# Kernel tuning notes

Hardware: AMD Instinct MI355X
Metric: run time of the kernel (lower is better)

Reference implementation:

```python
import jax, jax.numpy as jnp
import numpy as np

B, N = 4096, 1024


def setup_inputs() -> dict:
    key = jax.random.key(0)
    k1, k2 = jax.random.split(key)
    cors = 0.1 * jax.random.normal(k1, (B, N, 3), dtype=jnp.float32)  # predicted correspondences/offsets
    p_src = jax.random.normal(k2, (B, N, 3), dtype=jnp.float32)       # source point cloud
    return {"cors": cors, "p_src": p_src}


def reference(cors, p_src):
    # p_pred = p_src + cors  (target points implied by correspondences)
    p_pred = p_src + cors
    # centroids over the point dimension: [B, 1, 3]
    src_centroid = jnp.mean(p_src, axis=1, keepdims=True)
    pred_centroid = jnp.mean(p_pred, axis=1, keepdims=True)
    src_trans = p_src - src_centroid
    pred_trans = p_pred - pred_centroid
    # 3x3 cross-covariance per batch: h = src_trans^T @ pred_trans  -> [B, 3, 3]
    h = jnp.einsum('bnd,bne->bde', src_trans, pred_trans)
    # tf.linalg.svd returns s, u, v with h = u diag(s) v^T; jnp returns u, s, vh with vh = v^T
    u, s, vh = jnp.linalg.svd(h, full_matrices=False)
    # r_est = v @ u^T = (u @ vh)^T
    r_est = jnp.swapaxes(jnp.matmul(u, vh), -1, -2)  # [B, 3, 3]
    # t_est = -r_est @ src_centroid^T + pred_centroid^T  -> [B, 3, 1]
    t_est = -jnp.matmul(r_est, jnp.swapaxes(src_centroid, -1, -2)) + jnp.swapaxes(pred_centroid, -1, -2)
    g_top = jnp.concatenate([r_est, t_est], axis=2)  # [B, 3, 4]
    last_row = jnp.broadcast_to(
        jnp.array([[[0.0, 0.0, 0.0, 1.0]]], dtype=g_top.dtype), (g_top.shape[0], 1, 4)
    )
    return jnp.concatenate([g_top, last_row], axis=1)  # [B, 4, 4]
```

## Files before the change

### kernel.cpp

```cpp
#include <hip/hip_runtime.h>


constexpr int NPTS    = 1024;
constexpr int THREADS = 256;

__global__ __launch_bounds__(THREADS) void svd_layer_kernel(
    const float* __restrict__ cors,
    const float* __restrict__ p_src,
    float* __restrict__ out)
{
    const int b   = blockIdx.x;
    const int tid = threadIdx.x;
    const size_t base = (size_t)b * NPTS * 3;

    const float4* src4 = reinterpret_cast<const float4*>(p_src + base);
    const float4* cor4 = reinterpret_cast<const float4*>(cors  + base);
    float4 s0 = src4[tid*3+0], s1 = src4[tid*3+1], s2 = src4[tid*3+2];
    float4 c0 = cor4[tid*3+0], c1 = cor4[tid*3+1], c2 = cor4[tid*3+2];

    float sx[4] = {s0.x, s0.w, s1.z, s2.y};
    float sy[4] = {s0.y, s1.x, s1.w, s2.z};
    float sz[4] = {s0.z, s1.y, s2.x, s2.w};
    float px[4] = {sx[0]+c0.x, sx[1]+c0.w, sx[2]+c1.z, sx[3]+c2.y};
    float py[4] = {sy[0]+c0.y, sy[1]+c1.x, sy[2]+c1.w, sy[3]+c2.z};
    float pz[4] = {sz[0]+c0.z, sz[1]+c1.y, sz[2]+c2.x, sz[3]+c2.w};

    float acc[15];
    #pragma unroll
    for (int i = 0; i < 15; ++i) acc[i] = 0.f;
    #pragma unroll
    for (int k = 0; k < 4; ++k) {
        acc[0]  += sx[k]; acc[1]  += sy[k]; acc[2]  += sz[k];
        acc[3]  += px[k]; acc[4]  += py[k]; acc[5]  += pz[k];
        acc[6]  += sx[k]*px[k]; acc[7]  += sx[k]*py[k]; acc[8]  += sx[k]*pz[k];
        acc[9]  += sy[k]*px[k]; acc[10] += sy[k]*py[k]; acc[11] += sy[k]*pz[k];
        acc[12] += sz[k]*px[k]; acc[13] += sz[k]*py[k]; acc[14] += sz[k]*pz[k];
    }

    #pragma unroll
    for (int off = 32; off > 0; off >>= 1) {
        #pragma unroll
        for (int i = 0; i < 15; ++i) acc[i] += __shfl_down(acc[i], off, 64);
    }

    __shared__ float red[4][15];
    const int wave = tid >> 6, lane = tid & 63;
    if (lane == 0) {
        #pragma unroll
        for (int i = 0; i < 15; ++i) red[wave][i] = acc[i];
    }
    __syncthreads();
    if (tid != 0) return;

    double S[15];
    #pragma unroll
    for (int i = 0; i < 15; ++i)
        S[i] = (double)red[0][i] + (double)red[1][i] + (double)red[2][i] + (double)red[3][i];

    const double invN = 1.0 / (double)NPTS;
    double cs[3] = {S[0]*invN, S[1]*invN, S[2]*invN};
    double cp[3] = {S[3]*invN, S[4]*invN, S[5]*invN};

    double H[3][3];
    for (int i = 0; i < 3; ++i)
        for (int j = 0; j < 3; ++j)
            H[i][j] = S[6 + i*3 + j] - (double)NPTS * cs[i] * cp[j];

    double A[3][3];
    for (int i = 0; i < 3; ++i)
        for (int j = 0; j < 3; ++j) {
            double v = 0.0;
            for (int k = 0; k < 3; ++k) v += H[k][i] * H[k][j];
            A[i][j] = v;
        }

    double V[3][3] = {{1,0,0},{0,1,0},{0,0,1}};
    for (int sweep = 0; sweep < 8; ++sweep) {
        for (int pi = 0; pi < 3; ++pi) {
            const int p = (pi == 2) ? 1 : 0;
            const int q = (pi == 0) ? 1 : 2;
            const double apq = A[p][q];
            if (fabs(apq) < 1e-300) continue;
            const double tau = (A[q][q] - A[p][p]) / (2.0 * apq);
            const double t   = ((tau >= 0.0) ? 1.0 : -1.0) /
                               (fabs(tau) + sqrt(1.0 + tau*tau));
            const double c   = 1.0 / sqrt(1.0 + t*t);
            const double s   = t * c;
            A[p][p] -= t * apq;
            A[q][q] += t * apq;
            A[p][q] = A[q][p] = 0.0;
            const int k = 3 - p - q;
            const double akp = A[k][p], akq = A[k][q];
            A[k][p] = A[p][k] = c*akp - s*akq;
            A[k][q] = A[q][k] = s*akp + c*akq;
            for (int r = 0; r < 3; ++r) {
                const double vrp = V[r][p], vrq = V[r][q];
                V[r][p] = c*vrp - s*vrq;
                V[r][q] = s*vrp + c*vrq;
            }
        }
    }

    double inv[3];
    for (int i = 0; i < 3; ++i) {
        double w = A[i][i] > 0.0 ? A[i][i] : 0.0;
        double sv = sqrt(w);
        inv[i] = (sv > 1e-12) ? 1.0 / sv : 0.0;
    }
    double M[3][3];
    for (int i = 0; i < 3; ++i)
        for (int j = 0; j < 3; ++j) {
            double v = 0.0;
            for (int k = 0; k < 3; ++k) v += V[i][k] * inv[k] * V[j][k];
            M[i][j] = v;
        }

    double R[3][3];
    for (int i = 0; i < 3; ++i)
        for (int j = 0; j < 3; ++j) {
            double v = 0.0;
            for (int k = 0; k < 3; ++k) v += M[i][k] * H[j][k];
            R[i][j] = v;
        }
    double tt[3];
    for (int i = 0; i < 3; ++i)
        tt[i] = cp[i] - (R[i][0]*cs[0] + R[i][1]*cs[1] + R[i][2]*cs[2]);

    float* o = out + (size_t)b * 16;
    o[0]  = (float)R[0][0]; o[1]  = (float)R[0][1]; o[2]  = (float)R[0][2]; o[3]  = (float)tt[0];
    o[4]  = (float)R[1][0]; o[5]  = (float)R[1][1]; o[6]  = (float)R[1][2]; o[7]  = (float)tt[1];
    o[8]  = (float)R[2][0]; o[9]  = (float)R[2][1]; o[10] = (float)R[2][2]; o[11] = (float)tt[2];
    o[12] = 0.f; o[13] = 0.f; o[14] = 0.f; o[15] = 1.f;
}

extern "C" void kernel_launch(void* const* d_in, const int* in_sizes, int n_in,
                              void* d_out, int out_size, void* d_ws, size_t ws_size,
                              hipStream_t stream)
{
    const float* cors  = (const float*)d_in[0];
    const float* p_src = (const float*)d_in[1];
    float* out = (float*)d_out;
    const int B = in_sizes[0] / (NPTS * 3);
    hipLaunchKernelGGL(svd_layer_kernel, dim3(B), dim3(THREADS), 0, stream,
                       cors, p_src, out);
}
```

Baseline: 127.5 us.

## Map one batch per wavefront and replace Jacobi SVD with Newton-Schulz polar iteration

```diff
diff --git a/kernel.cpp b/kernel.cpp
--- a/kernel.cpp
+++ b/kernel.cpp
@@ -1,40 +1,53 @@
 #include <hip/hip_runtime.h>
 
 
-constexpr int NPTS    = 1024;
-constexpr int THREADS = 256;
+constexpr int NPTS  = 1024;
+constexpr int WAVES = 4;
+constexpr int THREADS = WAVES * 64;
 
 __global__ __launch_bounds__(THREADS) void svd_layer_kernel(
     const float* __restrict__ cors,
     const float* __restrict__ p_src,
-    float* __restrict__ out)
+    float* __restrict__ out,
+    int B)
 {
-    const int b   = blockIdx.x;
-    const int tid = threadIdx.x;
-    const size_t base = (size_t)b * NPTS * 3;
+    const int wave = threadIdx.x >> 6;
+    const int lane = threadIdx.x & 63;
+    const int b    = blockIdx.x * WAVES + wave;
+    if (b >= B) return;
 
-    const float4* src4 = reinterpret_cast<const float4*>(p_src + base);
-    const float4* cor4 = reinterpret_cast<const float4*>(cors  + base);
-    float4 s0 = src4[tid*3+0], s1 = src4[tid*3+1], s2 = src4[tid*3+2];
-    float4 c0 = cor4[tid*3+0], c1 = cor4[tid*3+1], c2 = cor4[tid*3+2];
+    const size_t base4 = (size_t)b * (NPTS * 3 / 4);
+    const float4* s4 = reinterpret_cast<const float4*>(p_src) + base4 + lane * 12;
+    const float4* c4 = reinterpret_cast<const float4*>(cors)  + base4 + lane * 12;
 
-    float sx[4] = {s0.x, s0.w, s1.z, s2.y};
-    float sy[4] = {s0.y, s1.x, s1.w, s2.z};
-    float sz[4] = {s0.z, s1.y, s2.x, s2.w};
-    float px[4] = {sx[0]+c0.x, sx[1]+c0.w, sx[2]+c1.z, sx[3]+c2.y};
-    float py[4] = {sy[0]+c0.y, sy[1]+c1.x, sy[2]+c1.w, sy[3]+c2.z};
-    float pz[4] = {sz[0]+c0.z, sz[1]+c1.y, sz[2]+c2.x, sz[3]+c2.w};
+    float4 sv[12], cv[12];
+    #pragma unroll
+    for (int m = 0; m < 12; ++m) sv[m] = s4[m];
+    #pragma unroll
+    for (int m = 0; m < 12; ++m) cv[m] = c4[m];
 
     float acc[15];
     #pragma unroll
     for (int i = 0; i < 15; ++i) acc[i] = 0.f;
+
     #pragma unroll
-    for (int k = 0; k < 4; ++k) {
-        acc[0]  += sx[k]; acc[1]  += sy[k]; acc[2]  += sz[k];
-        acc[3]  += px[k]; acc[4]  += py[k]; acc[5]  += pz[k];
-        acc[6]  += sx[k]*px[k]; acc[7]  += sx[k]*py[k]; acc[8]  += sx[k]*pz[k];
-        acc[9]  += sy[k]*px[k]; acc[10] += sy[k]*py[k]; acc[11] += sy[k]*pz[k];
-        acc[12] += sz[k]*px[k]; acc[13] += sz[k]*py[k]; acc[14] += sz[k]*pz[k];
+    for (int g = 0; g < 4; ++g) {
+        const float4 t0 = sv[g*3+0], t1 = sv[g*3+1], t2 = sv[g*3+2];
+        const float4 u0 = cv[g*3+0], u1 = cv[g*3+1], u2 = cv[g*3+2];
+        const float sx[4] = {t0.x, t0.w, t1.z, t2.y};
+        const float sy[4] = {t0.y, t1.x, t1.w, t2.z};
+        const float sz[4] = {t0.z, t1.y, t2.x, t2.w};
+        const float px[4] = {sx[0]+u0.x, sx[1]+u0.w, sx[2]+u1.z, sx[3]+u2.y};
+        const float py[4] = {sy[0]+u0.y, sy[1]+u1.x, sy[2]+u1.w, sy[3]+u2.z};
+        const float pz[4] = {sz[0]+u0.z, sz[1]+u1.y, sz[2]+u2.x, sz[3]+u2.w};
+        #pragma unroll
+        for (int k = 0; k < 4; ++k) {
+            acc[0]  += sx[k]; acc[1]  += sy[k]; acc[2]  += sz[k];
+            acc[3]  += px[k]; acc[4]  += py[k]; acc[5]  += pz[k];
+            acc[6]  += sx[k]*px[k]; acc[7]  += sx[k]*py[k]; acc[8]  += sx[k]*pz[k];
+            acc[9]  += sy[k]*px[k]; acc[10] += sy[k]*py[k]; acc[11] += sy[k]*pz[k];
+            acc[12] += sz[k]*px[k]; acc[13] += sz[k]*py[k]; acc[14] += sz[k]*pz[k];
+        }
     }
 
     #pragma unroll
@@ -43,94 +56,79 @@
         for (int i = 0; i < 15; ++i) acc[i] += __shfl_down(acc[i], off, 64);
     }
 
-    __shared__ float red[4][15];
-    const int wave = tid >> 6, lane = tid & 63;
-    if (lane == 0) {
+    if (lane != 0) return;
+
+    const float invN = 1.0f / (float)NPTS;
+    const float cs[3] = {acc[0]*invN, acc[1]*invN, acc[2]*invN};
+    const float cp[3] = {acc[3]*invN, acc[4]*invN, acc[5]*invN};
+
+    float Hm[3][3];
+    #pragma unroll
+    for (int i = 0; i < 3; ++i)
         #pragma unroll
-        for (int i = 0; i < 15; ++i) red[wave][i] = acc[i];
-    }
-    __syncthreads();
-    if (tid != 0) return;
+        for (int j = 0; j < 3; ++j)
+            Hm[i][j] = acc[6 + i*3 + j] - (float)NPTS * cs[i] * cp[j];
 
-    double S[15];
+    float K[3][3];
     #pragma unroll
-    for (int i = 0; i < 15; ++i)
-        S[i] = (double)red[0][i] + (double)red[1][i] + (double)red[2][i] + (double)red[3][i];
+    for (int i = 0; i < 3; ++i)
+        #pragma unroll
+        for (int j = 0; j < 3; ++j)
+            K[i][j] = Hm[0][i]*Hm[0][j] + Hm[1][i]*Hm[1][j] + Hm[2][i]*Hm[2][j];
 
-    const double invN = 1.0 / (double)NPTS;
-    double cs[3] = {S[0]*invN, S[1]*invN, S[2]*invN};
-    double cp[3] = {S[3]*invN, S[4]*invN, S[5]*invN};
+    const float tr3 = (K[0][0] + K[1][1] + K[2][2]) * (1.0f/3.0f);
+    const float is  = 1.0f / fmaxf(tr3, 1e-30f);
 
-    double H[3][3];
+    float Y[3][3], Z[3][3];
+    #pragma unroll
     for (int i = 0; i < 3; ++i)
-        for (int j = 0; j < 3; ++j)
-            H[i][j] = S[6 + i*3 + j] - (double)NPTS * cs[i] * cp[j];
-
-    double A[3][3];
-    for (int i = 0; i < 3; ++i)
+        #pragma unroll
         for (int j = 0; j < 3; ++j) {
-            double v = 0.0;
-            for (int k = 0; k < 3; ++k) v += H[k][i] * H[k][j];
-            A[i][j] = v;
+            Y[i][j] = K[i][j] * is;
+            Z[i][j] = (i == j) ? 1.0f : 0.0f;
         }
 
-    double V[3][3] = {{1,0,0},{0,1,0},{0,0,1}};
-    for (int sweep = 0; sweep < 8; ++sweep) {
-        for (int pi = 0; pi < 3; ++pi) {
-            const int p = (pi == 2) ? 1 : 0;
-            const int q = (pi == 0) ? 1 : 2;
-            const double apq = A[p][q];
-            if (fabs(apq) < 1e-300) continue;
-            const double tau = (A[q][q] - A[p][p]) / (2.0 * apq);
-            const double t   = ((tau >= 0.0) ? 1.0 : -1.0) /
-                               (fabs(tau) + sqrt(1.0 + tau*tau));
-            const double c   = 1.0 / sqrt(1.0 + t*t);
-            const double s   = t * c;
-            A[p][p] -= t * apq;
-            A[q][q] += t * apq;
-            A[p][q] = A[q][p] = 0.0;
-            const int k = 3 - p - q;
-            const double akp = A[k][p], akq = A[k][q];
-            A[k][p] = A[p][k] = c*akp - s*akq;
-            A[k][q] = A[q][k] = s*akp + c*akq;
-            for (int r = 0; r < 3; ++r) {
-                const double vrp = V[r][p], vrq = V[r][q];
-                V[r][p] = c*vrp - s*vrq;
-                V[r][q] = s*vrp + c*vrq;
+    #pragma unroll
+    for (int it = 0; it < 6; ++it) {
+        float W[3][3];
+        #pragma unroll
+        for (int i = 0; i < 3; ++i)
+            #pragma unroll
+            for (int j = 0; j < 3; ++j) {
+                float w = Z[i][0]*Y[0][j] + Z[i][1]*Y[1][j] + Z[i][2]*Y[2][j];
+                W[i][j] = ((i == j) ? 1.5f : 0.0f) - 0.5f * w;
             }
-        }
+        float Yn[3][3], Zn[3][3];
+        #pragma unroll
+        for (int i = 0; i < 3; ++i)
+            #pragma unroll
+            for (int j = 0; j < 3; ++j) {
+                Yn[i][j] = Y[i][0]*W[0][j] + Y[i][1]*W[1][j] + Y[i][2]*W[2][j];
+                Zn[i][j] = W[i][0]*Z[0][j] + W[i][1]*Z[1][j] + W[i][2]*Z[2][j];
+            }
+        #pragma unroll
+        for (int i = 0; i < 3; ++i)
+            #pragma unroll
+            for (int j = 0; j < 3; ++j) { Y[i][j] = Yn[i][j]; Z[i][j] = Zn[i][j]; }
     }
 
-    double inv[3];
-    for (int i = 0; i < 3; ++i) {
-        double w = A[i][i] > 0.0 ? A[i][i] : 0.0;
-        double sv = sqrt(w);
-        inv[i] = (sv > 1e-12) ? 1.0 / sv : 0.0;
-    }
-    double M[3][3];
+    const float rs = rsqrtf(fmaxf(tr3, 1e-30f));
+    float R[3][3];
+    #pragma unroll
     for (int i = 0; i < 3; ++i)
-        for (int j = 0; j < 3; ++j) {
-            double v = 0.0;
-            for (int k = 0; k < 3; ++k) v += V[i][k] * inv[k] * V[j][k];
-            M[i][j] = v;
-        }
+        #pragma unroll
+        for (int j = 0; j < 3; ++j)
+            R[i][j] = (Z[i][0]*Hm[j][0] + Z[i][1]*Hm[j][1] + Z[i][2]*Hm[j][2]) * rs;
 
-    double R[3][3];
-    for (int i = 0; i < 3; ++i)
-        for (int j = 0; j < 3; ++j) {
-            double v = 0.0;
-            for (int k = 0; k < 3; ++k) v += M[i][k] * H[j][k];
-            R[i][j] = v;
-        }
-    double tt[3];
-    for (int i = 0; i < 3; ++i)
-        tt[i] = cp[i] - (R[i][0]*cs[0] + R[i][1]*cs[1] + R[i][2]*cs[2]);
+    const float t0 = cp[0] - (R[0][0]*cs[0] + R[0][1]*cs[1] + R[0][2]*cs[2]);
+    const float t1 = cp[1] - (R[1][0]*cs[0] + R[1][1]*cs[1] + R[1][2]*cs[2]);
+    const float t2 = cp[2] - (R[2][0]*cs[0] + R[2][1]*cs[1] + R[2][2]*cs[2]);
 
-    float* o = out + (size_t)b * 16;
-    o[0]  = (float)R[0][0]; o[1]  = (float)R[0][1]; o[2]  = (float)R[0][2]; o[3]  = (float)tt[0];
-    o[4]  = (float)R[1][0]; o[5]  = (float)R[1][1]; o[6]  = (float)R[1][2]; o[7]  = (float)tt[1];
-    o[8]  = (float)R[2][0]; o[9]  = (float)R[2][1]; o[10] = (float)R[2][2]; o[11] = (float)tt[2];
-    o[12] = 0.f; o[13] = 0.f; o[14] = 0.f; o[15] = 1.f;
+    float4* o4 = reinterpret_cast<float4*>(out + (size_t)b * 16);
+    o4[0] = make_float4(R[0][0], R[0][1], R[0][2], t0);
+    o4[1] = make_float4(R[1][0], R[1][1], R[1][2], t1);
+    o4[2] = make_float4(R[2][0], R[2][1], R[2][2], t2);
+    o4[3] = make_float4(0.f, 0.f, 0.f, 1.f);
 }
 
 extern "C" void kernel_launch(void* const* d_in, const int* in_sizes, int n_in,
@@ -141,6 +139,7 @@
     const float* p_src = (const float*)d_in[1];
     float* out = (float*)d_out;
     const int B = in_sizes[0] / (NPTS * 3);
-    hipLaunchKernelGGL(svd_layer_kernel, dim3(B), dim3(THREADS), 0, stream,
-                       cors, p_src, out);
+    const int grid = (B + WAVES - 1) / WAVES;
+    hipLaunchKernelGGL(svd_layer_kernel, dim3(grid), dim3(THREADS), 0, stream,
+                       cors, p_src, out, B);
 }
```

Result: slower. 134.0 us (+5.1%).
